# Performance work log

Hardware: AMD Instinct MI355X
Metric: run time of the kernel (lower is better)

## Reference

```python
import jax, jax.numpy as jnp
import numpy as np

HIDDEN = 1024
ATTN = 1024
B, S = 4, 2048


def setup_inputs() -> dict:
    key = jax.random.key(0)
    ks = jax.random.split(key, 6)
    bound = 1.0 / np.sqrt(HIDDEN)
    return {
        "query": jax.random.normal(ks[0], (B, S, HIDDEN), jnp.float32),
        "value": jax.random.normal(ks[1], (B, S, HIDDEN), jnp.float32),
        "Wq": jax.random.uniform(ks[2], (HIDDEN, ATTN), jnp.float32, -bound, bound),
        "bq": jax.random.uniform(ks[3], (ATTN,), jnp.float32, -bound, bound),
        "Wv": jax.random.uniform(ks[4], (HIDDEN, ATTN), jnp.float32, -bound, bound),
        "bv": jax.random.uniform(ks[5], (ATTN,), jnp.float32, -bound, bound),
    }


def reference(query, value, Wq, bq, Wv, bv):
    # Linear projections (torch Linear: x @ W^T + b; here W stored as [in, out])
    q = jnp.einsum("bsh,hd->bsd", query, Wq) + bq  # [B,S,ATTN]
    v = jnp.einsum("bsh,hd->bsd", value, Wv) + bv  # [B,S,ATTN]
    # Unscaled dot-product attention
    scores = jnp.einsum("bqd,bkd->bqk", q, v)       # [B,S,S]
    attn = jax.nn.softmax(scores, axis=-1)
    context = jnp.einsum("bqk,bkd->bqd", attn, v)   # [B,S,ATTN]
    return context
```

## Files before the change

### kernel.cpp

```cpp
#include <hip/hip_runtime.h>
#include <hip/hip_bf16.h>


typedef unsigned short u16;
typedef __attribute__((ext_vector_type(8))) short bf16x8;
typedef __attribute__((ext_vector_type(4))) float f32x4;

typedef __attribute__((address_space(1))) void gvoid_t;
typedef __attribute__((address_space(3))) void svoid_t;

__device__ __forceinline__ void gll16(const void* g, void* l) {
    __builtin_amdgcn_global_load_lds((gvoid_t*)g, (svoid_t*)l, 16, 0, 0);
}

__device__ __forceinline__ u16 bf16rn(float x) {
    unsigned u = __float_as_uint(x);
    unsigned r = (u + 0x7FFFu + ((u >> 16) & 1u)) >> 16;
    return (u16)r;
}
__device__ __forceinline__ float bf2f(u16 h) {
    return __uint_as_float(((unsigned)h) << 16);
}

template<bool SPLITA, bool BIAS, bool OUTF32>
__global__ __launch_bounds__(256)
void gemm_mfma(const u16* __restrict__ Ah, const u16* __restrict__ Al,
               const u16* __restrict__ Bh, const u16* __restrict__ Bl,
               const float* __restrict__ bias,
               float* __restrict__ Of, u16* __restrict__ Ohi, u16* __restrict__ Olo,
               int M, int N, int K, long sA, long sB, long sC)
{
    __shared__ __align__(16) u16 sm[SPLITA ? 16384 : 12288];
    u16* Ash = sm;
    u16* Asl = SPLITA ? sm + 4096 : (u16*)nullptr;
    u16* Bsh = sm + (SPLITA ? 8192 : 4096);
    u16* Bsl = sm + (SPLITA ? 12288 : 8192);

    const long zb = blockIdx.z;
    Ah += zb * sA; if (SPLITA) Al += zb * sA;
    Bh += zb * sB; Bl += zb * sB;

    const int t = threadIdx.x, lane = t & 63, wv = t >> 6;
    const int wr = wv >> 1, wc = wv & 1;
    const int m0 = blockIdx.y << 7, n0 = blockIdx.x << 7;

    const int srow = (wv << 1) * 16 + (lane >> 2);
    const int scol = (lane & 3) << 4;

    const char* pAh0 = (const char*)(Ah + (long)(m0 + srow) * K) + scol;
    const char* pAh1 = pAh0 + (long)16 * K * 2;
    const char* pAl0 = SPLITA ? (const char*)(Al + (long)(m0 + srow) * K) + scol : nullptr;
    const char* pAl1 = SPLITA ? pAl0 + (long)16 * K * 2 : nullptr;
    const char* pBh0 = (const char*)(Bh + (long)(n0 + srow) * K) + scol;
    const char* pBh1 = pBh0 + (long)16 * K * 2;
    const char* pBl0 = (const char*)(Bl + (long)(n0 + srow) * K) + scol;
    const char* pBl1 = pBl0 + (long)16 * K * 2;

    u16* lAh0 = Ash + wv * 1024; u16* lAh1 = lAh0 + 512;
    u16* lAl0 = SPLITA ? Asl + wv * 1024 : (u16*)nullptr;
    u16* lAl1 = SPLITA ? lAl0 + 512 : (u16*)nullptr;
    u16* lBh0 = Bsh + wv * 1024; u16* lBh1 = lBh0 + 512;
    u16* lBl0 = Bsl + wv * 1024; u16* lBl1 = lBl0 + 512;

    const int afo = (wr * 64 + (lane & 15)) * 32 + (lane >> 4) * 8;
    const int bfo = (wc * 64 + (lane & 15)) * 32 + (lane >> 4) * 8;

    f32x4 acc[4][4];
#pragma unroll
    for (int i = 0; i < 4; ++i)
#pragma unroll
        for (int j = 0; j < 4; ++j) acc[i][j] = (f32x4)0.f;

    for (int k0 = 0; k0 < K; k0 += 32) {
        gll16(pAh0, lAh0); gll16(pAh1, lAh1);
        if (SPLITA) { gll16(pAl0, lAl0); gll16(pAl1, lAl1); }
        gll16(pBh0, lBh0); gll16(pBh1, lBh1);
        gll16(pBl0, lBl0); gll16(pBl1, lBl1);
        pAh0 += 64; pAh1 += 64; pBh0 += 64; pBh1 += 64; pBl0 += 64; pBl1 += 64;
        if (SPLITA) { pAl0 += 64; pAl1 += 64; }
        __syncthreads();

        bf16x8 ah[4], bh[4], bl[4];
#pragma unroll
        for (int i = 0; i < 4; ++i) {
            ah[i] = *(const bf16x8*)(Ash + afo + i * 512);
            bh[i] = *(const bf16x8*)(Bsh + bfo + i * 512);
            bl[i] = *(const bf16x8*)(Bsl + bfo + i * 512);
        }
#pragma unroll
        for (int i = 0; i < 4; ++i)
#pragma unroll
            for (int j = 0; j < 4; ++j)
                acc[i][j] = __builtin_amdgcn_mfma_f32_16x16x32_bf16(ah[i], bh[j], acc[i][j], 0, 0, 0);
#pragma unroll
        for (int i = 0; i < 4; ++i)
#pragma unroll
            for (int j = 0; j < 4; ++j)
                acc[i][j] = __builtin_amdgcn_mfma_f32_16x16x32_bf16(ah[i], bl[j], acc[i][j], 0, 0, 0);
        if (SPLITA) {
            bf16x8 al[4];
#pragma unroll
            for (int i = 0; i < 4; ++i) al[i] = *(const bf16x8*)(Asl + afo + i * 512);
#pragma unroll
            for (int i = 0; i < 4; ++i)
#pragma unroll
                for (int j = 0; j < 4; ++j)
                    acc[i][j] = __builtin_amdgcn_mfma_f32_16x16x32_bf16(al[i], bh[j], acc[i][j], 0, 0, 0);
        }
        __syncthreads();
    }

    float bcol[4] = {0, 0, 0, 0};
    if (BIAS) {
#pragma unroll
        for (int j = 0; j < 4; ++j)
            bcol[j] = bias[n0 + wc * 64 + j * 16 + (lane & 15)];
    }
#pragma unroll
    for (int i = 0; i < 4; ++i) {
#pragma unroll
        for (int j = 0; j < 4; ++j) {
            const int col = n0 + wc * 64 + j * 16 + (lane & 15);
            const int row0 = m0 + wr * 64 + i * 16 + ((lane >> 4) << 2);
#pragma unroll
            for (int r = 0; r < 4; ++r) {
                float x = acc[i][j][r] + bcol[j];
                long o = zb * sC + (long)(row0 + r) * N + col;
                if (OUTF32) {
                    Of[o] = x;
                } else {
                    u16 h = bf16rn(x);
                    Ohi[o] = h;
                    Olo[o] = bf16rn(x - bf2f(h));
                }
            }
        }
    }
}

__global__ __launch_bounds__(256)
void split_f32(const float* __restrict__ in, u16* __restrict__ hi, u16* __restrict__ lo)
{
    long i = ((long)blockIdx.x * 256 + threadIdx.x) * 4;
    float4 v = *(const float4*)(in + i);
    ushort4 h, l;
    h.x = bf16rn(v.x); l.x = bf16rn(v.x - bf2f(h.x));
    h.y = bf16rn(v.y); l.y = bf16rn(v.y - bf2f(h.y));
    h.z = bf16rn(v.z); l.z = bf16rn(v.z - bf2f(h.z));
    h.w = bf16rn(v.w); l.w = bf16rn(v.w - bf2f(h.w));
    *(ushort4*)(hi + i) = h;
    *(ushort4*)(lo + i) = l;
}

__global__ __launch_bounds__(256)
void tsplit_w(const float* __restrict__ W, u16* __restrict__ hi, u16* __restrict__ lo)
{
    __shared__ float tile[32][33];
    const int n0v = blockIdx.x * 32, k0 = blockIdx.y * 32;
    const int r = threadIdx.x >> 5, c = threadIdx.x & 31;
#pragma unroll
    for (int it = 0; it < 4; ++it)
        tile[r + it * 8][c] = W[(long)(k0 + r + it * 8) * 1024 + n0v + c];
    __syncthreads();
#pragma unroll
    for (int it = 0; it < 4; ++it) {
        const int rr = r + it * 8;
        float x = tile[c][rr];
        u16 h = bf16rn(x);
        long o = (long)(n0v + rr) * 1024 + k0 + c;
        hi[o] = h;
        lo[o] = bf16rn(x - bf2f(h));
    }
}

__global__ __launch_bounds__(256)
void tr_bf16(const u16* __restrict__ src, u16* __restrict__ dst)
{
    __shared__ u16 tile[32][33];
    src += (long)blockIdx.z * 2048 * 1024;
    dst += (long)blockIdx.z * 1024 * 2048;
    const int s0 = blockIdx.x * 32, d0 = blockIdx.y * 32;
    const int r = threadIdx.x >> 5, c = threadIdx.x & 31;
#pragma unroll
    for (int it = 0; it < 4; ++it)
        tile[r + it * 8][c] = src[(long)(s0 + r + it * 8) * 1024 + d0 + c];
    __syncthreads();
#pragma unroll
    for (int it = 0; it < 4; ++it) {
        const int rr = r + it * 8;
        dst[(long)(d0 + rr) * 2048 + s0 + c] = tile[c][rr];
    }
}

__global__ __launch_bounds__(256)
void softmax_p(const float* __restrict__ S, u16* __restrict__ P)
{
    const float* p = S + (long)blockIdx.x * 2048;
    u16* o = P + (long)blockIdx.x * 2048;
    const int t = threadIdx.x;

    float4 x0 = *(const float4*)&p[t * 4];
    float4 x1 = *(const float4*)&p[1024 + t * 4];

    float mx = fmaxf(fmaxf(fmaxf(x0.x, x0.y), fmaxf(x0.z, x0.w)),
                     fmaxf(fmaxf(x1.x, x1.y), fmaxf(x1.z, x1.w)));
#pragma unroll
    for (int off = 32; off; off >>= 1) mx = fmaxf(mx, __shfl_xor(mx, off));

    __shared__ float red[8];
    if ((t & 63) == 0) red[t >> 6] = mx;
    __syncthreads();
    mx = fmaxf(fmaxf(red[0], red[1]), fmaxf(red[2], red[3]));

    x0.x = __expf(x0.x - mx); x0.y = __expf(x0.y - mx);
    x0.z = __expf(x0.z - mx); x0.w = __expf(x0.w - mx);
    x1.x = __expf(x1.x - mx); x1.y = __expf(x1.y - mx);
    x1.z = __expf(x1.z - mx); x1.w = __expf(x1.w - mx);

    float sm2 = (x0.x + x0.y + x0.z + x0.w) + (x1.x + x1.y + x1.z + x1.w);
#pragma unroll
    for (int off = 32; off; off >>= 1) sm2 += __shfl_xor(sm2, off);
    if ((t & 63) == 0) red[4 + (t >> 6)] = sm2;
    __syncthreads();
    sm2 = (red[4] + red[5]) + (red[6] + red[7]);

    const float inv = 1.0f / sm2;
    ushort4 y;
    y.x = bf16rn(x0.x * inv); y.y = bf16rn(x0.y * inv);
    y.z = bf16rn(x0.z * inv); y.w = bf16rn(x0.w * inv);
    *(ushort4*)(o + t * 4) = y;
    y.x = bf16rn(x1.x * inv); y.y = bf16rn(x1.y * inv);
    y.z = bf16rn(x1.z * inv); y.w = bf16rn(x1.w * inv);
    *(ushort4*)(o + 1024 + t * 4) = y;
}

extern "C" void kernel_launch(void* const* d_in, const int* in_sizes, int n_in,
                              void* d_out, int out_size, void* d_ws, size_t ws_size,
                              hipStream_t stream)
{
    const float* query = (const float*)d_in[0];
    const float* value = (const float*)d_in[1];
    const float* Wq    = (const float*)d_in[2];
    const float* bq    = (const float*)d_in[3];
    const float* Wv    = (const float*)d_in[4];
    const float* bv    = (const float*)d_in[5];
    float* out = (float*)d_out;

    char* W = (char*)d_ws;
    u16* qx_hi = (u16*)(W);
    u16* qx_lo = qx_hi + 8388608;
    u16* vx_hi = qx_lo + 8388608;
    u16* vx_lo = vx_hi + 8388608;
    float* sc  = (float*)W;
    u16* q_hi  = (u16*)(W + 67108864);
    u16* q_lo  = q_hi + 8388608;
    u16* p     = (u16*)(W + 67108864);
    u16* v_hi  = (u16*)(W + 100663296);
    u16* v_lo  = v_hi + 8388608;
    u16* vT_hi = (u16*)(W + 134217728);
    u16* vT_lo = vT_hi + 8388608;
    u16* WqT_hi = (u16*)(W + 167772160);
    u16* WqT_lo = WqT_hi + 1048576;
    u16* WvT_hi = WqT_lo + 1048576;
    u16* WvT_lo = WvT_hi + 1048576;

    split_f32<<<8192, 256, 0, stream>>>(query, qx_hi, qx_lo);
    split_f32<<<8192, 256, 0, stream>>>(value, vx_hi, vx_lo);
    tsplit_w<<<dim3(32, 32), 256, 0, stream>>>(Wq, WqT_hi, WqT_lo);
    tsplit_w<<<dim3(32, 32), 256, 0, stream>>>(Wv, WvT_hi, WvT_lo);

    gemm_mfma<true, true, false><<<dim3(8, 64, 1), 256, 0, stream>>>(
        qx_hi, qx_lo, WqT_hi, WqT_lo, bq, nullptr, q_hi, q_lo,
        8192, 1024, 1024, 0, 0, 0);
    gemm_mfma<true, true, false><<<dim3(8, 64, 1), 256, 0, stream>>>(
        vx_hi, vx_lo, WvT_hi, WvT_lo, bv, nullptr, v_hi, v_lo,
        8192, 1024, 1024, 0, 0, 0);

    tr_bf16<<<dim3(64, 32, 4), 256, 0, stream>>>(v_hi, vT_hi);
    tr_bf16<<<dim3(64, 32, 4), 256, 0, stream>>>(v_lo, vT_lo);

    gemm_mfma<true, false, true><<<dim3(16, 16, 4), 256, 0, stream>>>(
        q_hi, q_lo, v_hi, v_lo, nullptr, sc, nullptr, nullptr,
        2048, 2048, 1024, 2048L * 1024, 2048L * 1024, 2048L * 2048);

    softmax_p<<<8192, 256, 0, stream>>>(sc, p);

    gemm_mfma<false, false, true><<<dim3(8, 16, 4), 256, 0, stream>>>(
        p, nullptr, vT_hi, vT_lo, nullptr, out, nullptr, nullptr,
        2048, 1024, 2048, 2048L * 2048, 1024L * 2048, 2048L * 1024);
}
```

Measured before the change: 462.8 us.

## Add pipelined 256x256 split-bf16 GEMM kernel for projections and scores

Adds a new 512-thread GEMM with 256x256 tiles, double-buffered LDS filled by async global-to-LDS loads, XOR-swizzled LDS layout, explicit waitcnt/barrier phasing and setprio around MFMA bursts. The three split-precision products (hi*hi, hi*lo, lo*hi) are folded into one concatenated K=3072 loop. The Q and V projections are merged into a single batched launch, and the QK^T scores GEMM also uses the new kernel. The goal is better MFMA utilization and less global traffic per FLOP. The cost is heavy register and LDS use, 128KB of dynamic shared memory, and hardcoded sizes that only fit this problem.

Result: faster. 441.7 us (-4.6%).

```diff
diff --git a/kernel.cpp b/kernel.cpp
--- a/kernel.cpp
+++ b/kernel.cpp
@@ -22,23 +22,179 @@
     return __uint_as_float(((unsigned)h) << 16);
 }
 
-template<bool SPLITA, bool BIAS, bool OUTF32>
+__device__ __forceinline__ const char* sel3(const char* p0, const char* p1,
+                                            const char* p2, int i) {
+    return i == 0 ? p0 : (i == 1 ? p1 : p2);
+}
+
+#define NSK 48
+
+#define STAGE_A(T, mh) {                                                      \
+    const char* _p = sel3(A0z, A1z, A2z, (T) >> 4) + (long)((T) & 15) * 128;  \
+    char* _d = smem + (((T) & 1) << 16) + ((mh) << 14) + (w << 10);           \
+    gll16(_p + offA##mh##0, _d);                                              \
+    gll16(_p + offA##mh##1, _d + 8192); }
+
+#define STAGE_B(T, nh) {                                                      \
+    const char* _p = sel3(B0z, B1z, B2z, (T) >> 4) + (long)((T) & 15) * 128;  \
+    char* _d = smem + (((T) & 1) << 16) + 32768 + ((nh) << 14) + (w << 10);   \
+    gll16(_p + offB##nh##0, _d);                                              \
+    gll16(_p + offB##nh##1, _d + 8192); }
+
+#define VM4 { asm volatile("s_waitcnt vmcnt(4)" ::: "memory");                \
+              __builtin_amdgcn_sched_barrier(0); }
+#define VM0 { asm volatile("s_waitcnt vmcnt(0)" ::: "memory");                \
+              __builtin_amdgcn_sched_barrier(0); }
+
+#define PHASE(mh, nh, STAGE, ENDW)                                            \
+  {                                                                           \
+    if ((nh) == 0) {                                                          \
+      _Pragma("unroll") for (int mi = 0; mi < 4; ++mi)                        \
+        _Pragma("unroll") for (int ks = 0; ks < 2; ++ks)                      \
+          afr[mi][ks] = *(const bf16x8*)(smem + bufb + ((mh) << 14) +         \
+              aRdB + mi * 2048 + csw[ks]);                                    \
+    }                                                                         \
+    bf16x8 bfr[2][2];                                                         \
+    _Pragma("unroll") for (int ni = 0; ni < 2; ++ni)                          \
+      _Pragma("unroll") for (int ks = 0; ks < 2; ++ks)                        \
+        bfr[ni][ks] = *(const bf16x8*)(smem + bufb + ((nh) << 14) +           \
+            bRdB + ni * 2048 + csw[ks]);                                      \
+    STAGE;                                                                    \
+    __builtin_amdgcn_s_barrier();                                             \
+    asm volatile("s_waitcnt lgkmcnt(0)" ::: "memory");                        \
+    __builtin_amdgcn_sched_barrier(0);                                        \
+    __builtin_amdgcn_s_setprio(1);                                            \
+    _Pragma("unroll") for (int mi = 0; mi < 4; ++mi)                          \
+      _Pragma("unroll") for (int ni = 0; ni < 2; ++ni)                        \
+        _Pragma("unroll") for (int ks = 0; ks < 2; ++ks)                      \
+          acc[(mh) * 4 + mi][(nh) * 2 + ni] =                                 \
+              __builtin_amdgcn_mfma_f32_16x16x32_bf16(                        \
+                  afr[mi][ks], bfr[ni][ks],                                   \
+                  acc[(mh) * 4 + mi][(nh) * 2 + ni], 0, 0, 0);                \
+    __builtin_amdgcn_s_setprio(0);                                            \
+    ENDW;                                                                     \
+    __builtin_amdgcn_s_barrier();                                             \
+  }
+
+template<bool OUTF32>
+__global__ __launch_bounds__(512, 2)
+void gemm8(const char* a0, const char* a1, const char* a2, long zA,
+           const char* b0, const char* b1, const char* b2, long zB,
+           float* __restrict__ Of, u16* __restrict__ Ohi, u16* __restrict__ Olo,
+           long zC, const float* __restrict__ bias0,
+           const float* __restrict__ bias1, int N)
+{
+    extern __shared__ char smem[];
+    const int t = threadIdx.x, lane = t & 63, w = t >> 6;
+    const int wm = w >> 2, wn = w & 3;
+    const int n0 = blockIdx.x << 8, m0 = blockIdx.y << 8;
+    const int z = blockIdx.z;
+
+    const char* A0z = a0 + (long)z * zA;
+    const char* A1z = a1 + (long)z * zA;
+    const char* A2z = a2 + (long)z * zA;
+    const char* B0z = b0 + (long)z * zB;
+    const char* B1z = b1 + (long)z * zB;
+    const char* B2z = b2 + (long)z * zB;
+
+    const int lr0 = t >> 3;
+    const long cg = (long)((((t & 7) ^ ((t >> 3) & 7)) << 4));
+    const long offA00 = (long)(m0 + lr0) * 2048 + cg;
+    const long offA01 = offA00 + 128L * 2048;
+    const long offA10 = (long)(m0 + 64 + lr0) * 2048 + cg;
+    const long offA11 = offA10 + 128L * 2048;
+    const long offB00 = (long)(n0 + ((lr0 >> 5) << 6) + (lr0 & 31)) * 2048 + cg;
+    const long offB01 = offB00 + 128L * 2048;
+    const long offB10 = offB00 + 32L * 2048;
+    const long offB11 = offB10 + 128L * 2048;
+
+    const int swl = (lane & 7) << 4;
+    const int csw[2] = { (((lane >> 4) << 4)) ^ swl,
+                         (((lane >> 4) << 4) + 64) ^ swl };
+    const int aRdB = (wm * 64 + (lane & 15)) * 128;
+    const int bRdB = 32768 + (wn * 32 + (lane & 15)) * 128;
+
+    f32x4 acc[8][4];
+#pragma unroll
+    for (int i = 0; i < 8; ++i)
+#pragma unroll
+        for (int j = 0; j < 4; ++j) acc[i][j] = (f32x4)0.f;
+    bf16x8 afr[4][2];
+
+    STAGE_A(0, 0); STAGE_B(0, 0); STAGE_A(0, 1); STAGE_B(0, 1);
+    STAGE_A(1, 0); STAGE_B(1, 0);
+    asm volatile("s_waitcnt vmcnt(4)" ::: "memory");
+    __builtin_amdgcn_sched_barrier(0);
+    __builtin_amdgcn_s_barrier();
+
+    for (int s = 0; s < NSK - 2; ++s) {
+        const int bufb = (s & 1) << 16;
+        PHASE(0, 0, STAGE_A(s + 1, 1), );
+        PHASE(0, 1, STAGE_B(s + 1, 1), );
+        PHASE(1, 0, STAGE_A(s + 2, 0), );
+        PHASE(1, 1, STAGE_B(s + 2, 0), VM4);
+    }
+    {
+        const int bufb = ((NSK - 2) & 1) << 16;
+        PHASE(0, 0, STAGE_A(NSK - 1, 1), );
+        PHASE(0, 1, STAGE_B(NSK - 1, 1), );
+        PHASE(1, 0, , );
+        PHASE(1, 1, , VM0);
+    }
+    {
+        const int bufb = ((NSK - 1) & 1) << 16;
+        PHASE(0, 0, , );
+        PHASE(0, 1, , );
+        PHASE(1, 0, , );
+        PHASE(1, 1, , );
+    }
+
+    const int r0 = m0 + wm * 128 + ((lane >> 4) << 2);
+    const int c0 = n0 + wn * 64 + (lane & 15);
+    if (OUTF32) {
+        float* Co = Of + (long)z * zC;
+#pragma unroll
+        for (int mi = 0; mi < 8; ++mi)
+#pragma unroll
+            for (int nj = 0; nj < 4; ++nj)
+#pragma unroll
+                for (int r = 0; r < 4; ++r)
+                    Co[(long)(r0 + mi * 16 + r) * N + c0 + nj * 16] =
+                        acc[mi][nj][r];
+    } else {
+        const float* bs = z ? bias1 : bias0;
+        float bc[4];
+#pragma unroll
+        for (int nj = 0; nj < 4; ++nj) bc[nj] = bs[c0 + nj * 16];
+        u16* Oh = Ohi + (long)z * zC;
+        u16* Ol = Olo + (long)z * zC;
+#pragma unroll
+        for (int mi = 0; mi < 8; ++mi)
+#pragma unroll
+            for (int nj = 0; nj < 4; ++nj)
+#pragma unroll
+                for (int r = 0; r < 4; ++r) {
+                    float x = acc[mi][nj][r] + bc[nj];
+                    long o = (long)(r0 + mi * 16 + r) * N + c0 + nj * 16;
+                    u16 h = bf16rn(x);
+                    Oh[o] = h;
+                    Ol[o] = bf16rn(x - bf2f(h));
+                }
+    }
+}
+
 __global__ __launch_bounds__(256)
-void gemm_mfma(const u16* __restrict__ Ah, const u16* __restrict__ Al,
-               const u16* __restrict__ Bh, const u16* __restrict__ Bl,
-               const float* __restrict__ bias,
-               float* __restrict__ Of, u16* __restrict__ Ohi, u16* __restrict__ Olo,
-               int M, int N, int K, long sA, long sB, long sC)
-{
-    __shared__ __align__(16) u16 sm[SPLITA ? 16384 : 12288];
+void gemm_pv(const u16* __restrict__ Ah, const u16* __restrict__ Bh,
+             const u16* __restrict__ Bl, float* __restrict__ Of,
+             int N, int K, long sA, long sB, long sC)
+{
+    __shared__ __align__(16) u16 sm[12288];
     u16* Ash = sm;
-    u16* Asl = SPLITA ? sm + 4096 : (u16*)nullptr;
-    u16* Bsh = sm + (SPLITA ? 8192 : 4096);
-    u16* Bsl = sm + (SPLITA ? 12288 : 8192);
+    u16* Bsh = sm + 4096;
+    u16* Bsl = sm + 8192;
 
     const long zb = blockIdx.z;
-    Ah += zb * sA; if (SPLITA) Al += zb * sA;
-    Bh += zb * sB; Bl += zb * sB;
+    Ah += zb * sA; Bh += zb * sB; Bl += zb * sB;
 
     const int t = threadIdx.x, lane = t & 63, wv = t >> 6;
     const int wr = wv >> 1, wc = wv & 1;
@@ -49,16 +205,12 @@
 
     const char* pAh0 = (const char*)(Ah + (long)(m0 + srow) * K) + scol;
     const char* pAh1 = pAh0 + (long)16 * K * 2;
-    const char* pAl0 = SPLITA ? (const char*)(Al + (long)(m0 + srow) * K) + scol : nullptr;
-    const char* pAl1 = SPLITA ? pAl0 + (long)16 * K * 2 : nullptr;
     const char* pBh0 = (const char*)(Bh + (long)(n0 + srow) * K) + scol;
     const char* pBh1 = pBh0 + (long)16 * K * 2;
     const char* pBl0 = (const char*)(Bl + (long)(n0 + srow) * K) + scol;
     const char* pBl1 = pBl0 + (long)16 * K * 2;
 
     u16* lAh0 = Ash + wv * 1024; u16* lAh1 = lAh0 + 512;
-    u16* lAl0 = SPLITA ? Asl + wv * 1024 : (u16*)nullptr;
-    u16* lAl1 = SPLITA ? lAl0 + 512 : (u16*)nullptr;
     u16* lBh0 = Bsh + wv * 1024; u16* lBh1 = lBh0 + 512;
     u16* lBl0 = Bsl + wv * 1024; u16* lBl1 = lBl0 + 512;
 
@@ -73,11 +225,9 @@
 
     for (int k0 = 0; k0 < K; k0 += 32) {
         gll16(pAh0, lAh0); gll16(pAh1, lAh1);
-        if (SPLITA) { gll16(pAl0, lAl0); gll16(pAl1, lAl1); }
         gll16(pBh0, lBh0); gll16(pBh1, lBh1);
         gll16(pBl0, lBl0); gll16(pBl1, lBl1);
         pAh0 += 64; pAh1 += 64; pBh0 += 64; pBh1 += 64; pBl0 += 64; pBl1 += 64;
-        if (SPLITA) { pAl0 += 64; pAl1 += 64; }
         __syncthreads();
 
         bf16x8 ah[4], bh[4], bl[4];
@@ -97,45 +247,19 @@
 #pragma unroll
             for (int j = 0; j < 4; ++j)
                 acc[i][j] = __builtin_amdgcn_mfma_f32_16x16x32_bf16(ah[i], bl[j], acc[i][j], 0, 0, 0);
-        if (SPLITA) {
-            bf16x8 al[4];
-#pragma unroll
-            for (int i = 0; i < 4; ++i) al[i] = *(const bf16x8*)(Asl + afo + i * 512);
-#pragma unroll
-            for (int i = 0; i < 4; ++i)
-#pragma unroll
-                for (int j = 0; j < 4; ++j)
-                    acc[i][j] = __builtin_amdgcn_mfma_f32_16x16x32_bf16(al[i], bh[j], acc[i][j], 0, 0, 0);
-        }
         __syncthreads();
     }
 
-    float bcol[4] = {0, 0, 0, 0};
-    if (BIAS) {
-#pragma unroll
-        for (int j = 0; j < 4; ++j)
-            bcol[j] = bias[n0 + wc * 64 + j * 16 + (lane & 15)];
-    }
-#pragma unroll
-    for (int i = 0; i < 4; ++i) {
+#pragma unroll
+    for (int i = 0; i < 4; ++i)
 #pragma unroll
         for (int j = 0; j < 4; ++j) {
             const int col = n0 + wc * 64 + j * 16 + (lane & 15);
             const int row0 = m0 + wr * 64 + i * 16 + ((lane >> 4) << 2);
 #pragma unroll
-            for (int r = 0; r < 4; ++r) {
-                float x = acc[i][j][r] + bcol[j];
-                long o = zb * sC + (long)(row0 + r) * N + col;
-                if (OUTF32) {
-                    Of[o] = x;
-                } else {
-                    u16 h = bf16rn(x);
-                    Ohi[o] = h;
-                    Olo[o] = bf16rn(x - bf2f(h));
-                }
-            }
+            for (int r = 0; r < 4; ++r)
+                Of[zb * sC + (long)(row0 + r) * N + col] = acc[i][j][r];
         }
-    }
 }
 
 __global__ __launch_bounds__(256)
@@ -264,28 +388,32 @@
     u16* WvT_hi = WqT_lo + 1048576;
     u16* WvT_lo = WvT_hi + 1048576;
 
+    hipFuncSetAttribute((const void*)&gemm8<false>,
+                        hipFuncAttributeMaxDynamicSharedMemorySize, 131072);
+    hipFuncSetAttribute((const void*)&gemm8<true>,
+                        hipFuncAttributeMaxDynamicSharedMemorySize, 131072);
+
     split_f32<<<8192, 256, 0, stream>>>(query, qx_hi, qx_lo);
     split_f32<<<8192, 256, 0, stream>>>(value, vx_hi, vx_lo);
     tsplit_w<<<dim3(32, 32), 256, 0, stream>>>(Wq, WqT_hi, WqT_lo);
     tsplit_w<<<dim3(32, 32), 256, 0, stream>>>(Wv, WvT_hi, WvT_lo);
 
-    gemm_mfma<true, true, false><<<dim3(8, 64, 1), 256, 0, stream>>>(
-        qx_hi, qx_lo, WqT_hi, WqT_lo, bq, nullptr, q_hi, q_lo,
-        8192, 1024, 1024, 0, 0, 0);
-    gemm_mfma<true, true, false><<<dim3(8, 64, 1), 256, 0, stream>>>(
-        vx_hi, vx_lo, WvT_hi, WvT_lo, bv, nullptr, v_hi, v_lo,
-        8192, 1024, 1024, 0, 0, 0);
+    gemm8<false><<<dim3(4, 32, 2), 512, 131072, stream>>>(
+        (const char*)qx_hi, (const char*)qx_hi, (const char*)qx_lo, 33554432L,
+        (const char*)WqT_hi, (const char*)WqT_lo, (const char*)WqT_hi, 4194304L,
+        nullptr, q_hi, q_lo, 16777216L, bq, bv, 1024);
 
     tr_bf16<<<dim3(64, 32, 4), 256, 0, stream>>>(v_hi, vT_hi);
     tr_bf16<<<dim3(64, 32, 4), 256, 0, stream>>>(v_lo, vT_lo);
 
-    gemm_mfma<true, false, true><<<dim3(16, 16, 4), 256, 0, stream>>>(
-        q_hi, q_lo, v_hi, v_lo, nullptr, sc, nullptr, nullptr,
-        2048, 2048, 1024, 2048L * 1024, 2048L * 1024, 2048L * 2048);
+    gemm8<true><<<dim3(8, 8, 4), 512, 131072, stream>>>(
+        (const char*)q_hi, (const char*)q_hi, (const char*)q_lo, 4194304L,
+        (const char*)v_hi, (const char*)v_lo, (const char*)v_hi, 4194304L,
+        sc, nullptr, nullptr, 4194304L, nullptr, nullptr, 2048);
 
     softmax_p<<<8192, 256, 0, stream>>>(sc, p);
 
-    gemm_mfma<false, false, true><<<dim3(8, 16, 4), 256, 0, stream>>>(
-        p, nullptr, vT_hi, vT_lo, nullptr, out, nullptr, nullptr,
-        2048, 1024, 2048, 2048L * 2048, 1024L * 2048, 2048L * 1024);
-}
+    gemm_pv<<<dim3(8, 16, 4), 256, 0, stream>>>(
+        p, vT_hi, vT_lo, out,
+        1024, 2048, 2048L * 2048, 1024L * 2048, 2048L * 1024);
+}
```
